# Kernel tuning notes

Measured on AMD Instinct MI355X. Metric: run time of the kernel, lower is better.

## Reference

```python
import jax, jax.numpy as jnp
import numpy as np

N, LQ, D_MODEL, M_HEADS, P_POINTS, H_DIM, W_DIM = 8, 4096, 256, 8, 4, 64, 64


def setup_inputs() -> dict:
    key = jax.random.key(0)
    ks = jax.random.split(key, 9)
    d = D_MODEL
    scale = 1.0 / np.sqrt(d).astype(np.float32)
    return {
        "query": jax.random.normal(ks[0], (N, LQ, d), jnp.float32),
        "reference_points": jax.random.uniform(ks[1], (N, LQ, 2), jnp.float32),
        "input_flatten": jax.random.normal(ks[2], (N, H_DIM * W_DIM, d), jnp.float32),
        "H": H_DIM,
        "W": W_DIM,
        "Wv": jax.random.normal(ks[3], (d, d), jnp.float32) * scale,
        "bv": jnp.zeros((d,), jnp.float32),
        "Woff": jax.random.normal(ks[4], (M_HEADS * P_POINTS * 2, d), jnp.float32) * 0.01,
        "boff": jax.random.normal(ks[5], (M_HEADS * P_POINTS * 2,), jnp.float32) * 0.5,
        "Wa": jax.random.normal(ks[6], (M_HEADS * P_POINTS, d), jnp.float32) * 0.01,
        "ba": jnp.zeros((M_HEADS * P_POINTS,), jnp.float32),
        "Wo": jax.random.normal(ks[7], (d, d), jnp.float32) * scale,
        "bo": jnp.zeros((d,), jnp.float32),
    }


def _bilinear_sample(val, grid, H, W):
    # val: [B, D, H*W]; grid: [B, Lq, P, 2] in [-1, 1] (x, y); align_corners=False, zero padding.
    B, D, _ = val.shape
    _, Lq, P, _ = grid.shape
    x = (grid[..., 0] + 1.0) * (W * 0.5) - 0.5
    y = (grid[..., 1] + 1.0) * (H * 0.5) - 0.5
    x0 = jnp.floor(x)
    y0 = jnp.floor(y)
    x0i = x0.astype(jnp.int32)
    y0i = y0.astype(jnp.int32)
    wx1 = x - x0
    wy1 = y - y0
    out = jnp.zeros((B, D, Lq, P), val.dtype)
    for xi, wx in ((x0i, 1.0 - wx1), (x0i + 1, wx1)):
        for yi, wy in ((y0i, 1.0 - wy1), (y0i + 1, wy1)):
            valid = (xi >= 0) & (xi < W) & (yi >= 0) & (yi < H)
            idx = jnp.clip(yi, 0, H - 1) * W + jnp.clip(xi, 0, W - 1)  # [B, Lq, P]
            g = jnp.take_along_axis(val, idx.reshape(B, 1, Lq * P), axis=2).reshape(B, D, Lq, P)
            w = jnp.where(valid, wx * wy, 0.0)
            out = out + g * w[:, None]
    return out


def reference(query, reference_points, input_flatten, H, W, Wv, bv, Woff, boff, Wa, ba, Wo, bo):
    n, lq, d = query.shape
    m, p = M_HEADS, P_POINTS
    dh = d // m
    value = (input_flatten @ Wv.T + bv).reshape(n, H * W, m, dh)
    offsets = (query @ Woff.T + boff).reshape(n, lq, m, p, 2)
    attw = jax.nn.softmax((query @ Wa.T + ba).reshape(n, lq, m, p), axis=-1)
    normalizer = jnp.array([W, H], dtype=query.dtype)  # [W, H] order per torch code
    loc = reference_points[:, :, None, None, :] + offsets / normalizer
    grid = 2.0 * loc - 1.0  # [n, lq, m, p, 2]
    # value -> [n*m, dh, H*W] matching torch flatten(2).transpose(1,2).reshape
    val = jnp.transpose(value, (0, 2, 3, 1)).reshape(n * m, dh, H * W)
    grd = jnp.transpose(grid, (0, 2, 1, 3, 4)).reshape(n * m, lq, p, 2)
    samp = _bilinear_sample(val, grd, H, W)  # [n*m, dh, lq, p]
    aw = jnp.transpose(attw, (0, 2, 1, 3)).reshape(n * m, 1, lq, p)
    out = (samp * aw).sum(-1).reshape(n, m * dh, lq)
    out = jnp.transpose(out, (0, 2, 1))  # [n, lq, d]
    return out @ Wo.T + bo
```

## Files before the change

kernel.cpp:

```cpp
#include <hip/hip_runtime.h>
#include <math.h>

#define NB   8
#define LQN  4096
#define DM   256
#define MH   8
#define PP   4
#define HH   64
#define WW   64
#define PW   67
#define PPIX (PW*PW)

typedef __bf16 bf16x8 __attribute__((ext_vector_type(8)));
typedef float  f32x4  __attribute__((ext_vector_type(4)));
typedef unsigned short us8 __attribute__((ext_vector_type(8)));
typedef unsigned short us4 __attribute__((ext_vector_type(4)));

__device__ __forceinline__ unsigned short f2bf(float f) {
    unsigned u = __float_as_uint(f);
    u += 0x7FFFu + ((u >> 16) & 1u);
    return (unsigned short)(u >> 16);
}
__device__ __forceinline__ float bf2f(unsigned short b) {
    return __uint_as_float((unsigned)b << 16);
}

__device__ __forceinline__ void gl2lds16(const void* g, unsigned short* l) {
    __builtin_amdgcn_global_load_lds(
        (const __attribute__((address_space(1))) void*)g,
        (__attribute__((address_space(3))) void*)l,
        16, 0, 0);
}

__device__ __forceinline__ bf16x8 cvt_frag(const unsigned short* s, int row, int kq) {
    const int u0 = row * 8 + ((kq * 2) ^ (row & 7));
    const int u1 = u0 ^ 1;
    const f32x4 a0 = *(const f32x4*)&s[u0 * 8];
    const f32x4 a1 = *(const f32x4*)&s[u1 * 8];
    bf16x8 v;
    v[0] = (__bf16)a0[0]; v[1] = (__bf16)a0[1];
    v[2] = (__bf16)a0[2]; v[3] = (__bf16)a0[3];
    v[4] = (__bf16)a1[0]; v[5] = (__bf16)a1[1];
    v[6] = (__bf16)a1[2]; v[7] = (__bf16)a1[3];
    return v;
}

__global__ __launch_bounds__(256)
void prep_kernel(const float* __restrict__ Wv, const float* __restrict__ Wo,
                 const float* __restrict__ Woff, const float* __restrict__ Wa,
                 const float* __restrict__ boff, const float* __restrict__ ba,
                 unsigned short* __restrict__ Wvh, unsigned short* __restrict__ Woh,
                 unsigned short* __restrict__ Wcath, float* __restrict__ bcat,
                 unsigned short* __restrict__ valueP) {
    const int i = blockIdx.x * 256 + threadIdx.x;
    if (i < 65536) {
        Wvh[i] = f2bf(Wv[i]);
    } else if (i < 131072) {
        const int j = i - 65536;
        Woh[j] = f2bf(Wo[j]);
    } else if (i < 163840) {
        const int j = i - 131072, n = j >> 8, k = j & 255;
        const float v = (n < 64) ? Woff[n * 256 + k]
                                 : ((n < 96) ? Wa[(n - 64) * 256 + k] : 0.f);
        Wcath[j] = f2bf(v);
    } else if (i < 163968) {
        const int n = i - 163840;
        bcat[n] = (n < 64) ? boff[n] : ((n < 96) ? ba[n - 64] : 0.f);
    } else if (i < 163968 + 201216) {
        const int j   = i - 163968;
        const int c4  = j & 63;
        const int pix = j >> 6;
        const int n   = pix / 393;
        const int r   = pix - n * 393;
        int x, y;
        if (r < 201) {
            const int q = r / 67;
            y = (q == 0) ? 0 : (q == 1 ? 65 : 66);
            x = r - q * 67;
        } else {
            const int q = r - 201;
            y = 1 + q / 3;
            const int s = q - (q / 3) * 3;
            x = (s == 0) ? 0 : (s == 1 ? 65 : 66);
        }
        const size_t addr = ((size_t)n * PPIX + (size_t)y * PW + x) * DM + c4 * 4;
        *(ushort4*)&valueP[addr] = make_ushort4(0, 0, 0, 0);
    }
}

__global__ __launch_bounds__(256, 4)
void value_gemm(const float* __restrict__ Ain,
                const unsigned short* __restrict__ Wvh,
                const float* __restrict__ bv,
                unsigned short* __restrict__ valueP) {
    constexpr int K = 256, NK = 8;
    __shared__ unsigned short sA[2][4096];
    __shared__ unsigned short sB[2][4096];

    const int t   = threadIdx.x;
    const int blk = blockIdx.x;
    const int xb  = blk & 7;
    const int idx = blk >> 3;
    const int brow = xb * 4096 + (idx >> 1) * 64;
    const int bcol = (idx & 1) * 128;

    const int srow = t >> 3;
    const int scq  = (t & 7) ^ (srow & 7);
    const float* aG = Ain + (size_t)(brow + srow) * K + scq * 4;
    const size_t aI = (size_t)32 * K;

    const unsigned short* bG = Wvh + (size_t)(bcol + (t >> 2)) * K + (t & 3) * 8;
    const size_t bI = (size_t)64 * K;

    const int l   = t & 63;
    const int wid = t >> 6;
    const int wr  = wid >> 1, wc = wid & 1;
    const int fr  = l & 15,   kq = l >> 4;

    f32x4 acc[2][4] = {};

#define STAGE(buf, ks_) { const int k0_ = (ks_) * 32;                    \
       gl2lds16(aG + k0_,      &sA[buf][t * 8]);                         \
       gl2lds16(aG + k0_ + aI, &sA[buf][2048 + t * 8]);                  \
       gl2lds16(bG + k0_,      &sB[buf][t * 8]);                         \
       gl2lds16(bG + k0_ + bI, &sB[buf][2048 + t * 8]); }

    STAGE(0, 0);
    STAGE(1, 1);

    for (int ks = 0; ks < NK; ++ks) {
        const int cur = ks & 1;
        if (ks < NK - 1) asm volatile("s_waitcnt vmcnt(4)" ::: "memory");
        else             asm volatile("s_waitcnt vmcnt(0)" ::: "memory");
        __builtin_amdgcn_s_barrier();
        __builtin_amdgcn_sched_barrier(0);

        bf16x8 af[2], bf_[4];
#pragma unroll
        for (int m = 0; m < 2; ++m)
            af[m]  = cvt_frag(sA[cur], wr * 32 + m * 16 + fr, kq);
#pragma unroll
        for (int n = 0; n < 4; ++n)
            bf_[n] = *(const bf16x8*)&sB[cur][(wc * 64 + n * 16 + fr) * 32 + kq * 8];

#pragma unroll
        for (int m = 0; m < 2; ++m)
#pragma unroll
            for (int n = 0; n < 4; ++n)
                acc[m][n] = __builtin_amdgcn_mfma_f32_16x16x32_bf16(
                    bf_[n], af[m], acc[m][n], 0, 0, 0);

        __builtin_amdgcn_sched_barrier(0);
        __builtin_amdgcn_s_barrier();
        if (ks + 2 < NK) STAGE(cur, ks + 2);
    }
#undef STAGE

#pragma unroll
    for (int m = 0; m < 2; ++m) {
        const int row = brow + wr * 32 + m * 16 + fr;
        const int nb_ = row >> 12;
        const int pix = row & 4095;
        const int y   = pix >> 6, x = pix & 63;
        const size_t rbase =
            ((size_t)nb_ * PPIX + (size_t)(y + 1) * PW + (x + 1)) * DM;
#pragma unroll
        for (int n = 0; n < 4; ++n) {
            const int colq = bcol + wc * 64 + n * 16 + kq * 4;
            const float4 b4 = *(const float4*)&bv[colq];
            us4 o;
            o[0] = f2bf(acc[m][n][0] + b4.x);
            o[1] = f2bf(acc[m][n][1] + b4.y);
            o[2] = f2bf(acc[m][n][2] + b4.z);
            o[3] = f2bf(acc[m][n][3] + b4.w);
            *(us4*)&valueP[rbase + colq] = o;
        }
    }
}

__global__ __launch_bounds__(512, 4)
void fused_lso(const float* __restrict__ query, const float* __restrict__ refp,
               const unsigned short* __restrict__ valueP,
               const unsigned short* __restrict__ Wcath,
               const float* __restrict__ bcat,
               const unsigned short* __restrict__ Woh,
               const float* __restrict__ bo, float* __restrict__ C) {
    constexpr int K = 256, NK = 8;
    extern __shared__ unsigned short smem[];
    unsigned short* sS = smem;
    unsigned short* sB = smem + 16384;
    unsigned short* sL = smem + 32768;

    const int t    = threadIdx.x;
    const int blk  = blockIdx.x;
    const int nb   = blk & 7;
    const int brow = nb * 4096 + (blk >> 3) * 64;
    const int w    = t >> 6;
    const int lane = t & 63;
    const int fr   = lane & 15, kq = lane >> 4;

    {
        unsigned short* sQ = sS;
        unsigned short* sW = sS + 8192;

        const int srow = t >> 3;
        const int scq  = (t & 7) ^ (srow & 7);
        const float* aG = query + (size_t)(brow + srow) * K + scq * 4;
        const unsigned short* wG = Wcath + (size_t)(t >> 2) * K + (t & 3) * 8;

        const int wr0 = w >> 2;
        const int wc0 = w & 3;

        f32x4 acc[2][2] = {};

#define STG0(buf, ks_) { const int k0_ = (ks_) * 32;                     \
       gl2lds16(aG + k0_, &sQ[(buf) * 4096 + t * 8]);                    \
       gl2lds16(wG + k0_, &sW[(buf) * 4096 + t * 8]); }

        STG0(0, 0);
        STG0(1, 1);

        for (int ks = 0; ks < NK; ++ks) {
            const int cur = ks & 1;
            if (ks < NK - 1) asm volatile("s_waitcnt vmcnt(2)" ::: "memory");
            else             asm volatile("s_waitcnt vmcnt(0)" ::: "memory");
            __builtin_amdgcn_s_barrier();
            __builtin_amdgcn_sched_barrier(0);

            bf16x8 af[2], bw[2];
#pragma unroll
            for (int m = 0; m < 2; ++m)
                af[m] = cvt_frag(&sQ[cur * 4096], wr0 * 32 + m * 16 + fr, kq);
#pragma unroll
            for (int n = 0; n < 2; ++n)
                bw[n] = *(const bf16x8*)&sW[cur * 4096 +
                        (wc0 * 32 + n * 16 + fr) * 32 + kq * 8];

#pragma unroll
            for (int m = 0; m < 2; ++m)
#pragma unroll
                for (int n = 0; n < 2; ++n)
                    acc[m][n] = __builtin_amdgcn_mfma_f32_16x16x32_bf16(
                        bw[n], af[m], acc[m][n], 0, 0, 0);

            __builtin_amdgcn_sched_barrier(0);
            __builtin_amdgcn_s_barrier();
            if (ks + 2 < NK) STG0(cur, ks + 2);
        }
#undef STG0

#pragma unroll
        for (int m = 0; m < 2; ++m) {
            const int row = wr0 * 32 + m * 16 + fr;
#pragma unroll
            for (int n = 0; n < 2; ++n) {
                const int colq = wc0 * 32 + n * 16 + kq * 4;
                const float4 b4 = *(const float4*)&bcat[colq];
                us4 o;
                o[0] = f2bf(acc[m][n][0] + b4.x);
                o[1] = f2bf(acc[m][n][1] + b4.y);
                o[2] = f2bf(acc[m][n][2] + b4.z);
                o[3] = f2bf(acc[m][n][3] + b4.w);
                *(us4*)&sL[row * 128 + colq] = o;
            }
        }
    }
    __syncthreads();

    {
        const int tp  = lane & 31;
        const int pm  = tp >> 2, ppt = tp & 3;
        const int half = lane >> 5;
        const int c8   = lane & 31;
        const int mh   = c8 >> 2;
        const unsigned short* vbase = valueP + (size_t)nb * (PPIX * DM) + c8 * 8;

        for (int i = 0; i < 8; i += 2) {
            const int qa = w * 8 + i;
            const int qb = qa + 1;

            us8 gA0[4], gB0[4]; float wA0[4], wB0[4];
            {
                const unsigned short* lg = sL + qa * 128;
                const int b = brow + qa;
                const float rx = refp[(size_t)b * 2 + 0];
                const float ry = refp[(size_t)b * 2 + 1];
                const float ox = bf2f(lg[pm * 8 + ppt * 2 + 0]);
                const float oy = bf2f(lg[pm * 8 + ppt * 2 + 1]);
                const float la = bf2f(lg[64 + tp]);
                const float x = fminf(fmaxf(fmaf(rx, (float)WW, ox) - 0.5f, -1.0f), 64.0f);
                const float y = fminf(fmaxf(fmaf(ry, (float)HH, oy) - 0.5f, -1.0f), 64.0f);
                float mx = fmaxf(la, __shfl_xor(la, 1));
                mx = fmaxf(mx, __shfl_xor(mx, 2));
                const float e = __expf(la - mx);
                float den = e + __shfl_xor(e, 1);
                den += __shfl_xor(den, 2);
                const float wgt = e / den;
#pragma unroll
                for (int p = 0; p < PP; ++p) {
                    const int   sl = mh * PP + p;
                    const float xp = __shfl(x, sl);
                    const float yp = __shfl(y, sl);
                    const float wp = __shfl(wgt, sl);
                    const float x0f = floorf(xp), y0f = floorf(yp);
                    const int   x0 = (int)x0f,   y0 = (int)y0f;
                    const float wx1 = xp - x0f,  wy1 = yp - y0f;
                    const float wy  = half ? wy1 : (1.f - wy1);
                    wA0[p] = wp * wy * (1.f - wx1);
                    wB0[p] = wp * wy * wx1;
                    const unsigned short* p0 =
                        vbase + (size_t)((y0 + 1 + half) * PW + (x0 + 1)) * DM;
                    gA0[p] = *(const us8*)(p0);
                    gB0[p] = *(const us8*)(p0 + DM);
                }
            }

            us8 gA1[4], gB1[4]; float wA1[4], wB1[4];
            {
                const unsigned short* lg = sL + qb * 128;
                const int b = brow + qb;
                const float rx = refp[(size_t)b * 2 + 0];
                const float ry = refp[(size_t)b * 2 + 1];
                const float ox = bf2f(lg[pm * 8 + ppt * 2 + 0]);
                const float oy = bf2f(lg[pm * 8 + ppt * 2 + 1]);
                const float la = bf2f(lg[64 + tp]);
                const float x = fminf(fmaxf(fmaf(rx, (float)WW, ox) - 0.5f, -1.0f), 64.0f);
                const float y = fminf(fmaxf(fmaf(ry, (float)HH, oy) - 0.5f, -1.0f), 64.0f);
                float mx = fmaxf(la, __shfl_xor(la, 1));
                mx = fmaxf(mx, __shfl_xor(mx, 2));
                const float e = __expf(la - mx);
                float den = e + __shfl_xor(e, 1);
                den += __shfl_xor(den, 2);
                const float wgt = e / den;
#pragma unroll
                for (int p = 0; p < PP; ++p) {
                    const int   sl = mh * PP + p;
                    const float xp = __shfl(x, sl);
                    const float yp = __shfl(y, sl);
                    const float wp = __shfl(wgt, sl);
                    const float x0f = floorf(xp), y0f = floorf(yp);
                    const int   x0 = (int)x0f,   y0 = (int)y0f;
                    const float wx1 = xp - x0f,  wy1 = yp - y0f;
                    const float wy  = half ? wy1 : (1.f - wy1);
                    wA1[p] = wp * wy * (1.f - wx1);
                    wB1[p] = wp * wy * wx1;
                    const unsigned short* p0 =
                        vbase + (size_t)((y0 + 1 + half) * PW + (x0 + 1)) * DM;
                    gA1[p] = *(const us8*)(p0);
                    gB1[p] = *(const us8*)(p0 + DM);
                }
            }

            {
                float accv[8] = {};
#pragma unroll
                for (int p = 0; p < PP; ++p)
#pragma unroll
                    for (int j = 0; j < 8; ++j) {
                        accv[j] = fmaf(wA0[p], bf2f(gA0[p][j]), accv[j]);
                        accv[j] = fmaf(wB0[p], bf2f(gB0[p][j]), accv[j]);
                    }
#pragma unroll
                for (int j = 0; j < 8; ++j)
                    accv[j] += __shfl_xor(accv[j], 32);
                if (half == 0) {
                    us8 o;
#pragma unroll
                    for (int j = 0; j < 8; ++j) o[j] = f2bf(accv[j]);
                    *(us8*)&sS[qa * 256 + ((c8 ^ (qa & 7)) * 8)] = o;
                }
            }
            {
                float accv[8] = {};
#pragma unroll
                for (int p = 0; p < PP; ++p)
#pragma unroll
                    for (int j = 0; j < 8; ++j) {
                        accv[j] = fmaf(wA1[p], bf2f(gA1[p][j]), accv[j]);
                        accv[j] = fmaf(wB1[p], bf2f(gB1[p][j]), accv[j]);
                    }
#pragma unroll
                for (int j = 0; j < 8; ++j)
                    accv[j] += __shfl_xor(accv[j], 32);
                if (half == 0) {
                    us8 o;
#pragma unroll
                    for (int j = 0; j < 8; ++j) o[j] = f2bf(accv[j]);
                    *(us8*)&sS[qb * 256 + ((c8 ^ (qb & 7)) * 8)] = o;
                }
            }
        }
    }
    __syncthreads();

    const unsigned short* bG = Woh + (size_t)(t >> 2) * K + (t & 3) * 8;
    const size_t rHalf = (size_t)128 * K;

    const int wr = w >> 2, wc = w & 3;

    f32x4 acc[2][4] = {};

#define STAGEF(buf, ks_) { const int k0_ = (ks_) * 32;                   \
       gl2lds16(bG + k0_,         &sB[(buf) * 8192 + t * 8]);            \
       gl2lds16(bG + k0_ + rHalf, &sB[(buf) * 8192 + 4096 + t * 8]); }

    STAGEF(0, 0);
    STAGEF(1, 1);

    for (int ks = 0; ks < NK; ++ks) {
        const int cur = ks & 1;
        if (ks < NK - 1) asm volatile("s_waitcnt vmcnt(2)" ::: "memory");
        else             asm volatile("s_waitcnt vmcnt(0)" ::: "memory");
        __builtin_amdgcn_s_barrier();
        __builtin_amdgcn_sched_barrier(0);

        bf16x8 af[2], bfr[4];
#pragma unroll
        for (int m = 0; m < 2; ++m) {
            const int row = wr * 32 + m * 16 + fr;
            const int u   = (ks * 4 + kq) ^ (row & 7);
            af[m] = *(const bf16x8*)&sS[row * 256 + u * 8];
        }
#pragma unroll
        for (int n = 0; n < 4; ++n)
            bfr[n] = *(const bf16x8*)&sB[cur * 8192 + (wc * 64 + n * 16 + fr) * 32 + kq * 8];

#pragma unroll
        for (int m = 0; m < 2; ++m)
#pragma unroll
            for (int n = 0; n < 4; ++n)
                acc[m][n] = __builtin_amdgcn_mfma_f32_16x16x32_bf16(
                    bfr[n], af[m], acc[m][n], 0, 0, 0);

        __builtin_amdgcn_sched_barrier(0);
        __builtin_amdgcn_s_barrier();
        if (ks + 2 < NK) STAGEF(cur, ks + 2);
    }
#undef STAGEF

#pragma unroll
    for (int m = 0; m < 2; ++m) {
        const int row = brow + wr * 32 + m * 16 + fr;
#pragma unroll
        for (int n = 0; n < 4; ++n) {
            const int colq = wc * 64 + n * 16 + kq * 4;
            const float4 bs = *(const float4*)&bo[colq];
            float4 o;
            o.x = acc[m][n][0] + bs.x; o.y = acc[m][n][1] + bs.y;
            o.z = acc[m][n][2] + bs.z; o.w = acc[m][n][3] + bs.w;
            *(float4*)&C[(size_t)row * DM + colq] = o;
        }
    }
}

extern "C" void kernel_launch(void* const* d_in, const int* in_sizes, int n_in,
                              void* d_out, int out_size, void* d_ws, size_t ws_size,
                              hipStream_t stream) {
    const float* query  = (const float*)d_in[0];
    const float* refp   = (const float*)d_in[1];
    const float* inputf = (const float*)d_in[2];
    const float* Wv   = (const float*)d_in[5];
    const float* bv   = (const float*)d_in[6];
    const float* Woff = (const float*)d_in[7];
    const float* boff = (const float*)d_in[8];
    const float* Wa   = (const float*)d_in[9];
    const float* ba   = (const float*)d_in[10];
    const float* Wo   = (const float*)d_in[11];
    const float* bo   = (const float*)d_in[12];
    float* out = (float*)d_out;

    unsigned short* valueP = (unsigned short*)d_ws;
    unsigned short* Wvh    = valueP + (size_t)NB * PPIX * DM;
    unsigned short* Woh    = Wvh    + 65536;
    unsigned short* Wcath  = Woh    + 65536;
    float*          bcat   = (float*)(Wcath + 32768);

    prep_kernel<<<1427, 256, 0, stream>>>(Wv, Wo, Woff, Wa, boff, ba,
                                          Wvh, Woh, Wcath, bcat, valueP);

    value_gemm<<<1024, 256, 0, stream>>>(inputf, Wvh, bv, valueP);

    fused_lso<<<512, 512, 81920, stream>>>(query, refp, valueP, Wcath, bcat,
                                           Woh, bo, out);
}
```

Before: 58.57 us.

## Shrink fused kernel LDS footprint to raise occupancy, single-buffer output weights

Cuts the fused kernel's dynamic LDS from 80KB to 48KB so more blocks can be resident. It does this by aliasing the sampling-offset buffer with the Wo staging buffer, storing only the 96 used logit columns at a 104-element stride, and dropping the Wo double-buffering. Launch bounds are raised to 6 blocks per CU. The cost is that output-GEMM weight loads are no longer overlapped with MFMA work, and register limits tighten.

```diff
diff --git a/kernel.cpp b/kernel.cpp
--- a/kernel.cpp
+++ b/kernel.cpp
@@ -10,6 +10,7 @@
 #define WW   64
 #define PW   67
 #define PPIX (PW*PW)
+#define LSTR 104
 
 typedef __bf16 bf16x8 __attribute__((ext_vector_type(8)));
 typedef float  f32x4  __attribute__((ext_vector_type(4)));
@@ -178,7 +179,7 @@
     }
 }
 
-__global__ __launch_bounds__(512, 4)
+__global__ __launch_bounds__(512, 6)
 void fused_lso(const float* __restrict__ query, const float* __restrict__ refp,
                const unsigned short* __restrict__ valueP,
                const unsigned short* __restrict__ Wcath,
@@ -188,8 +189,7 @@
     constexpr int K = 256, NK = 8;
     extern __shared__ unsigned short smem[];
     unsigned short* sS = smem;
-    unsigned short* sB = smem + 16384;
-    unsigned short* sL = smem + 32768;
+    unsigned short* sU = smem + 16384;
 
     const int t    = threadIdx.x;
     const int blk  = blockIdx.x;
@@ -202,6 +202,7 @@
     {
         unsigned short* sQ = sS;
         unsigned short* sW = sS + 8192;
+        unsigned short* sL = sU;
 
         const int srow = t >> 3;
         const int scq  = (t & 7) ^ (srow & 7);
@@ -255,19 +256,22 @@
 #pragma unroll
             for (int n = 0; n < 2; ++n) {
                 const int colq = wc0 * 32 + n * 16 + kq * 4;
-                const float4 b4 = *(const float4*)&bcat[colq];
-                us4 o;
-                o[0] = f2bf(acc[m][n][0] + b4.x);
-                o[1] = f2bf(acc[m][n][1] + b4.y);
-                o[2] = f2bf(acc[m][n][2] + b4.z);
-                o[3] = f2bf(acc[m][n][3] + b4.w);
-                *(us4*)&sL[row * 128 + colq] = o;
+                if (colq < 96) {
+                    const float4 b4 = *(const float4*)&bcat[colq];
+                    us4 o;
+                    o[0] = f2bf(acc[m][n][0] + b4.x);
+                    o[1] = f2bf(acc[m][n][1] + b4.y);
+                    o[2] = f2bf(acc[m][n][2] + b4.z);
+                    o[3] = f2bf(acc[m][n][3] + b4.w);
+                    *(us4*)&sL[row * LSTR + colq] = o;
+                }
             }
         }
     }
     __syncthreads();
 
     {
+        const unsigned short* sL = sU;
         const int tp  = lane & 31;
         const int pm  = tp >> 2, ppt = tp & 3;
         const int half = lane >> 5;
@@ -281,7 +285,7 @@
 
             us8 gA0[4], gB0[4]; float wA0[4], wB0[4];
             {
-                const unsigned short* lg = sL + qa * 128;
+                const unsigned short* lg = sL + qa * LSTR;
                 const int b = brow + qa;
                 const float rx = refp[(size_t)b * 2 + 0];
                 const float ry = refp[(size_t)b * 2 + 1];
@@ -317,7 +321,7 @@
 
             us8 gA1[4], gB1[4]; float wA1[4], wB1[4];
             {
-                const unsigned short* lg = sL + qb * 128;
+                const unsigned short* lg = sL + qb * LSTR;
                 const int b = brow + qb;
                 const float rx = refp[(size_t)b * 2 + 0];
                 const float ry = refp[(size_t)b * 2 + 1];
@@ -400,17 +404,14 @@
 
     f32x4 acc[2][4] = {};
 
-#define STAGEF(buf, ks_) { const int k0_ = (ks_) * 32;                   \
-       gl2lds16(bG + k0_,         &sB[(buf) * 8192 + t * 8]);            \
-       gl2lds16(bG + k0_ + rHalf, &sB[(buf) * 8192 + 4096 + t * 8]); }
-
-    STAGEF(0, 0);
-    STAGEF(1, 1);
+#define STAGEF(ks_) { const int k0_ = (ks_) * 32;                        \
+       gl2lds16(bG + k0_,         &sU[t * 8]);                           \
+       gl2lds16(bG + k0_ + rHalf, &sU[4096 + t * 8]); }
+
+    STAGEF(0);
 
     for (int ks = 0; ks < NK; ++ks) {
-        const int cur = ks & 1;
-        if (ks < NK - 1) asm volatile("s_waitcnt vmcnt(2)" ::: "memory");
-        else             asm volatile("s_waitcnt vmcnt(0)" ::: "memory");
+        asm volatile("s_waitcnt vmcnt(0)" ::: "memory");
         __builtin_amdgcn_s_barrier();
         __builtin_amdgcn_sched_barrier(0);
 
@@ -423,7 +424,7 @@
         }
 #pragma unroll
         for (int n = 0; n < 4; ++n)
-            bfr[n] = *(const bf16x8*)&sB[cur * 8192 + (wc * 64 + n * 16 + fr) * 32 + kq * 8];
+            bfr[n] = *(const bf16x8*)&sU[(wc * 64 + n * 16 + fr) * 32 + kq * 8];
 
 #pragma unroll
         for (int m = 0; m < 2; ++m)
@@ -434,7 +435,7 @@
 
         __builtin_amdgcn_sched_barrier(0);
         __builtin_amdgcn_s_barrier();
-        if (ks + 2 < NK) STAGEF(cur, ks + 2);
+        if (ks + 1 < NK) STAGEF(ks + 1);
     }
 #undef STAGEF
 
@@ -480,6 +481,6 @@
 
     value_gemm<<<1024, 256, 0, stream>>>(inputf, Wvh, bv, valueP);
 
-    fused_lso<<<512, 512, 81920, stream>>>(query, refp, valueP, Wcath, bcat,
+    fused_lso<<<512, 512, 49152, stream>>>(query, refp, valueP, Wcath, bcat,
                                            Woh, bo, out);
 }
```

Measured after the change: 64.77 us. 10.6% more time.
